# Kernel tuning notes

Hardware: AMD Instinct MI355X
Metric: run time of the kernel (lower is better)

Reference implementation:

```python
import jax, jax.numpy as jnp
import numpy as np

B, N, C, H, K = 4, 8192, 512, 8, 256
D = C // H  # head_dim = 64
EPS = 1e-6


def setup_inputs() -> dict:
    key = jax.random.key(0)
    k1, k2, k3 = jax.random.split(key, 3)
    x = jax.random.normal(k1, (B, N, C), dtype=jnp.float32)
    # Dense kernel (Keras default glorot-ish scale approximated; exact init irrelevant for math check)
    w_qkvv = jax.random.normal(k2, (C, 4 * C), dtype=jnp.float32) * (1.0 / np.sqrt(C))
    # UniformSqrtDim: uniform(-1/sqrt(K), 1/sqrt(K)) over shape (N, K)
    lim = 1.0 / np.sqrt(K)
    spatial_proj = jax.random.uniform(k3, (N, K), minval=-lim, maxval=lim, dtype=jnp.float32)
    temp_ca = jnp.ones((H, 1, 1), dtype=jnp.float32)
    temp_sa = jnp.ones((H, 1, 1), dtype=jnp.float32)
    return {"x": x, "w_qkvv": w_qkvv, "spatial_proj": spatial_proj,
            "temp_ca": temp_ca, "temp_sa": temp_sa}


def _safe_normalize(t):
    # normalize along last axis with clamped squared-sum (matches safe_normalize)
    sq = jnp.sum(t * t, axis=-1, keepdims=True)
    sq = jnp.where(sq < EPS, EPS, sq)
    return t / jnp.sqrt(sq)


def reference(x, w_qkvv, spatial_proj, temp_ca, temp_sa):
    b, n, c = x.shape
    qkvv = x @ w_qkvv  # [B, N, 4C]
    qkvv = qkvv.reshape(b, n, 4, H, D).transpose(2, 0, 3, 1, 4)  # [4, B, H, N, D]
    q, k, v_ca, v_sa = qkvv[0], qkvv[1], qkvv[2], qkvv[3]
    # transpose to [B, H, D, N]; normalize along N (tokens)
    q_t = q.transpose(0, 1, 3, 2)
    k_t = k.transpose(0, 1, 3, 2)
    v_ca_t = v_ca.transpose(0, 1, 3, 2)
    v_sa_t = v_sa.transpose(0, 1, 3, 2)
    q_norm = _safe_normalize(q_t)  # [B, H, D, N]
    k_norm = _safe_normalize(k_t)

    # --- Channel attention: [B,H,D,D] over small head_dim ---
    attn_ca = jnp.einsum('bhdn,bhen->bhde', q_norm, k_norm) * temp_ca
    attn_ca = jax.nn.softmax(attn_ca, axis=-1)
    x_ca = jnp.einsum('bhde,bhen->bhdn', attn_ca, v_ca_t)  # [B,H,D,N]
    x_ca = x_ca.transpose(0, 3, 1, 2).reshape(b, n, c)  # [B,N,C]

    # --- Spatial attention with N->K token projection ---
    k_proj = jnp.einsum('bhdn,nk->bhdk', k_norm, spatial_proj)  # [B,H,D,K]
    v_proj = jnp.einsum('bhdn,nk->bhdk', v_sa_t, spatial_proj)  # [B,H,D,K]
    attn_sa = jnp.einsum('bhdn,bhdk->bhnk', q_norm, k_proj) * temp_sa  # [B,H,N,K]
    attn_sa = jax.nn.softmax(attn_sa, axis=-1)
    x_sa = jnp.einsum('bhnk,bhdk->bhnd', attn_sa, v_proj)  # [B,H,N,D]
    x_sa = x_sa.transpose(0, 2, 1, 3).reshape(b, n, c)

    return x_ca + x_sa
```

## Files before the change

### kernel.cpp

```cpp
#include <hip/hip_runtime.h>
#include <hip/hip_bf16.h>

#define BATCH 4
#define SEQ   8192
#define CH    512
#define NHEAD 8
#define HDIM  64
#define KTOK  256
#define FOURC 2048

typedef __attribute__((ext_vector_type(8))) short bf16x8;
typedef __attribute__((ext_vector_type(4))) float f32x4;

#define GLOAD_LDS16(g, l)                                                      \
  __builtin_amdgcn_global_load_lds(                                            \
      (const __attribute__((address_space(1))) void*)(g),                      \
      (__attribute__((address_space(3))) void*)(l), 16, 0, 0)

__device__ __forceinline__ ushort bf16bits(float f) {
  __hip_bfloat16 b = __float2bfloat16(f);
  return *reinterpret_cast<ushort*>(&b);
}
__device__ __forceinline__ uint packbf2(float lo, float hi) {
  return (uint)bf16bits(lo) | ((uint)bf16bits(hi) << 16);
}

__global__ __launch_bounds__(256) void k_wt(
    const float* __restrict__ W, __hip_bfloat16* __restrict__ Wt) {
  __shared__ float tile[32][33];
  const int bx = blockIdx.x * 32;
  const int by = blockIdx.y * 32;
  const int t = threadIdx.x;
  const int r = t >> 5, c = t & 31;
#pragma unroll
  for (int it = 0; it < 4; ++it)
    tile[r + it * 8][c] = W[(size_t)(by + r + it * 8) * FOURC + bx + c];
  __syncthreads();
#pragma unroll
  for (int it = 0; it < 4; ++it) {
    int n = r + it * 8;
    Wt[(size_t)(bx + n) * CH + by + c] = __float2bfloat16(tile[c][n]);
  }
}

__global__ __launch_bounds__(256) void k_pt(
    const float* __restrict__ P, __hip_bfloat16* __restrict__ Pt) {
  __shared__ float tile[32][33];
  const int n0 = blockIdx.x * 32, k0 = blockIdx.y * 32;
  const int t = threadIdx.x, r = t >> 5, c = t & 31;
#pragma unroll
  for (int i = 0; i < 4; ++i)
    tile[r + i * 8][c] = P[(size_t)(n0 + r + i * 8) * KTOK + k0 + c];
  __syncthreads();
#pragma unroll
  for (int i = 0; i < 4; ++i)
    Pt[(size_t)(k0 + r + i * 8) * SEQ + n0 + c] = __float2bfloat16(tile[c][r + i * 8]);
}

__global__ __launch_bounds__(256) void k_xbf(
    const float* __restrict__ X, __hip_bfloat16* __restrict__ Xb) {
  size_t i = ((size_t)blockIdx.x * 256 + threadIdx.x) * 8;
  float4 a = *reinterpret_cast<const float4*>(&X[i]);
  float4 b = *reinterpret_cast<const float4*>(&X[i + 4]);
  ushort tmp[8];
  tmp[0] = bf16bits(a.x); tmp[1] = bf16bits(a.y);
  tmp[2] = bf16bits(a.z); tmp[3] = bf16bits(a.w);
  tmp[4] = bf16bits(b.x); tmp[5] = bf16bits(b.y);
  tmp[6] = bf16bits(b.z); tmp[7] = bf16bits(b.w);
  *reinterpret_cast<uint4*>(&Xb[i]) = *reinterpret_cast<const uint4*>(tmp);
}

__global__ __launch_bounds__(256) void k_gemm_mfma(
    const __hip_bfloat16* __restrict__ Xb, const __hip_bfloat16* __restrict__ Wt,
    __hip_bfloat16* __restrict__ QKVV) {
  __shared__ __align__(16) __hip_bfloat16 As[128 * 32];
  __shared__ __align__(16) __hip_bfloat16 Bs[128 * 32];
  const int t = threadIdx.x;
  const int wid = t >> 6, lane = t & 63;
  const int bid = blockIdx.x;
  const int xcd = bid & 7;
  const int l = bid >> 3;
  const int bm = (xcd * 32 + (l >> 4)) * 128;
  const int bn = (l & 15) * 128;
  const int wr = wid >> 1, wc = wid & 1;
  const int lrow = lane & 15;
  const int lk = (((lane >> 4) ^ ((lrow >> 1) & 3))) * 8;
  const int srow = lane >> 2;
  const int sk8 = (((lane & 3) ^ ((lane >> 3) & 3))) * 8;
  f32x4 acc[4][4] = {};
  for (int k0 = 0; k0 < CH; k0 += 32) {
#pragma unroll
    for (int i = 0; i < 2; ++i) {
      const int c = wid * 2 + i;
      GLOAD_LDS16(&Xb[(size_t)(bm + c * 16 + srow) * CH + k0 + sk8], &As[c * 512]);
      GLOAD_LDS16(&Wt[(size_t)(bn + c * 16 + srow) * CH + k0 + sk8], &Bs[c * 512]);
    }
    __syncthreads();
    bf16x8 af[4], bfr[4];
#pragma unroll
    for (int i = 0; i < 4; ++i)
      af[i] = *reinterpret_cast<const bf16x8*>(&As[(wr * 64 + i * 16 + lrow) * 32 + lk]);
#pragma unroll
    for (int j = 0; j < 4; ++j)
      bfr[j] = *reinterpret_cast<const bf16x8*>(&Bs[(wc * 64 + j * 16 + lrow) * 32 + lk]);
#pragma unroll
    for (int i = 0; i < 4; ++i)
#pragma unroll
      for (int j = 0; j < 4; ++j)
        acc[i][j] = __builtin_amdgcn_mfma_f32_16x16x32_bf16(af[i], bfr[j], acc[i][j], 0, 0, 0);
    __syncthreads();
  }
  const int l4 = (lane >> 4) * 4;
#pragma unroll
  for (int i = 0; i < 4; ++i)
#pragma unroll
    for (int j = 0; j < 4; ++j) {
      int col = bn + wc * 64 + j * 16 + lrow;
#pragma unroll
      for (int r = 0; r < 4; ++r) {
        int row = bm + wr * 64 + i * 16 + l4 + r;
        QKVV[(size_t)row * FOURC + col] = __float2bfloat16(acc[i][j][r]);
      }
    }
}

__global__ __launch_bounds__(256) void k_finalize(
    const float* __restrict__ sumsq, float* __restrict__ invq, float* __restrict__ invk) {
  int i = blockIdx.x * 256 + threadIdx.x;
  if (i < 2048) {
    invq[i] = rsqrtf(fmaxf(sumsq[i], 1e-6f));
    invk[i] = rsqrtf(fmaxf(sumsq[2048 + i], 1e-6f));
  }
}

__global__ __launch_bounds__(256) void k_qkstats(
    const __hip_bfloat16* __restrict__ QKVV,
    const __hip_bfloat16* __restrict__ Pt,
    float* __restrict__ G, float* __restrict__ sumsq, float* __restrict__ raw) {
  __shared__ __hip_bfloat16 qT[64][40];
  __shared__ __hip_bfloat16 kT[64][40];
  __shared__ __hip_bfloat16 vT[64][40];
  __shared__ __hip_bfloat16 pT[256][40];
  __shared__ float red[32][64];
  const int bh = blockIdx.y, b = bh >> 3, h = bh & 7;
  const int nbase = blockIdx.x * 1024;
  const int t = threadIdx.x, w = t >> 6, lane = t & 63;
  const int l15 = lane & 15, g = lane >> 4;
  const int comp = w >> 1, kh = w & 1;
  const int srow = t >> 3, sdq = (t & 7) * 8;
  f32x4 acc[4][8] = {};
  f32x4 accg[4] = {};
  float sqq[8] = {}, sqk[8] = {};
  for (int n0 = nbase; n0 < nbase + 1024; n0 += 32) {
    size_t gb = (size_t)(b * SEQ + n0 + srow) * FOURC + h * HDIM + sdq;
    uint4 uq = *reinterpret_cast<const uint4*>(&QKVV[gb]);
    uint4 uk = *reinterpret_cast<const uint4*>(&QKVV[gb + CH]);
    uint4 uv = *reinterpret_cast<const uint4*>(&QKVV[gb + 3 * CH]);
    const __hip_bfloat16* hq = reinterpret_cast<const __hip_bfloat16*>(&uq);
    const __hip_bfloat16* hk = reinterpret_cast<const __hip_bfloat16*>(&uk);
    const __hip_bfloat16* hv = reinterpret_cast<const __hip_bfloat16*>(&uv);
#pragma unroll
    for (int j = 0; j < 8; ++j) {
      float fq = __bfloat162float(hq[j]);
      float fk = __bfloat162float(hk[j]);
      sqq[j] = fmaf(fq, fq, sqq[j]);
      sqk[j] = fmaf(fk, fk, sqk[j]);
      qT[sdq + j][srow] = hq[j];
      kT[sdq + j][srow] = hk[j];
      vT[sdq + j][srow] = hv[j];
    }
#pragma unroll
    for (int ps = 0; ps < 4; ++ps) {
      int k = ps * 64 + (t >> 2);
      int poff = (t & 3) * 8;
      *reinterpret_cast<uint4*>(&pT[k][poff]) =
          *reinterpret_cast<const uint4*>(&Pt[(size_t)k * SEQ + n0 + poff]);
    }
    __syncthreads();
    {
      bf16x8 Aq[4];
#pragma unroll
      for (int dt = 0; dt < 4; ++dt)
        Aq[dt] = *reinterpret_cast<const bf16x8*>(&qT[dt * 16 + l15][g * 8]);
      bf16x8 Bk = *reinterpret_cast<const bf16x8*>(&kT[w * 16 + l15][g * 8]);
#pragma unroll
      for (int dt = 0; dt < 4; ++dt)
        accg[dt] = __builtin_amdgcn_mfma_f32_16x16x32_bf16(Aq[dt], Bk, accg[dt], 0, 0, 0);
    }
    {
      bf16x8 A[4], B[8];
#pragma unroll
      for (int dt = 0; dt < 4; ++dt)
        A[dt] = comp ? *reinterpret_cast<const bf16x8*>(&vT[dt * 16 + l15][g * 8])
                     : *reinterpret_cast<const bf16x8*>(&kT[dt * 16 + l15][g * 8]);
#pragma unroll
      for (int kt = 0; kt < 8; ++kt)
        B[kt] = *reinterpret_cast<const bf16x8*>(&pT[(kh * 8 + kt) * 16 + l15][g * 8]);
#pragma unroll
      for (int dt = 0; dt < 4; ++dt)
#pragma unroll
        for (int kt = 0; kt < 8; ++kt)
          acc[dt][kt] = __builtin_amdgcn_mfma_f32_16x16x32_bf16(A[dt], B[kt], acc[dt][kt], 0, 0, 0);
    }
    __syncthreads();
  }
#pragma unroll
  for (int j = 0; j < 8; ++j) red[srow][sdq + j] = sqq[j];
  __syncthreads();
  if (t < 64) {
    float tot = 0.f;
#pragma unroll
    for (int r = 0; r < 32; ++r) tot += red[r][t];
    atomicAdd(&sumsq[bh * 64 + t], tot);
  }
  __syncthreads();
#pragma unroll
  for (int j = 0; j < 8; ++j) red[srow][sdq + j] = sqk[j];
  __syncthreads();
  if (t < 64) {
    float tot = 0.f;
#pragma unroll
    for (int r = 0; r < 32; ++r) tot += red[r][t];
    atomicAdd(&sumsq[2048 + bh * 64 + t], tot);
  }
  float* gp = G + (size_t)bh * 4096;
#pragma unroll
  for (int dt = 0; dt < 4; ++dt)
#pragma unroll
    for (int r = 0; r < 4; ++r)
      atomicAdd(&gp[(dt * 16 + g * 4 + r) * 64 + w * 16 + l15], accg[dt][r]);
  float* rp = raw + ((size_t)bh * 2 + comp) * (64 * 256);
#pragma unroll
  for (int dt = 0; dt < 4; ++dt)
#pragma unroll
    for (int kt = 0; kt < 8; ++kt)
#pragma unroll
      for (int r = 0; r < 4; ++r)
        atomicAdd(&rp[(dt * 16 + g * 4 + r) * 256 + (kh * 8 + kt) * 16 + l15],
                  acc[dt][kt][r]);
}

__global__ __launch_bounds__(64) void k_ca_softmax(
    float* __restrict__ G, const float* __restrict__ invq,
    const float* __restrict__ invk, const float* __restrict__ tca) {
  const int bh = blockIdx.x, h = bh & 7;
  const int d = threadIdx.x;
  float* row = G + (size_t)bh * 4096 + d * 64;
  const float s0 = invq[bh * 64 + d] * tca[h];
  float vals[64];
  float m = -3.0e38f;
#pragma unroll
  for (int e = 0; e < 64; ++e) {
    float v = row[e] * s0 * invk[bh * 64 + e];
    vals[e] = v;
    m = fmaxf(m, v);
  }
  float s = 0.f;
#pragma unroll
  for (int e = 0; e < 64; ++e) { vals[e] = __expf(vals[e] - m); s += vals[e]; }
  float r = 1.0f / s;
#pragma unroll
  for (int e = 0; e < 64; ++e) row[e] = vals[e] * r;
}

__global__ __launch_bounds__(256) void k_projfin(
    const float* __restrict__ raw, const float* __restrict__ invq,
    const float* __restrict__ invk, const float* __restrict__ tsa,
    __hip_bfloat16* __restrict__ kpT, __hip_bfloat16* __restrict__ vpT) {
  const int bh = blockIdx.x, h = bh & 7;
  const int t = threadIdx.x;
  __shared__ float tile[64][65];
  const float ts = tsa[h];
  const float* r0 = raw + (size_t)bh * 2 * 16384;
  for (int kc = 0; kc < 4; ++kc) {
    for (int i = t; i < 4096; i += 256) {
      int d = i >> 6, kk = i & 63;
      tile[d][kk] = r0[d * 256 + kc * 64 + kk];
    }
    __syncthreads();
    for (int i = t; i < 4096; i += 256) {
      int kk = i >> 6, d = i & 63;
      float sc = invq[bh * 64 + d] * invk[bh * 64 + d] * ts;
      kpT[(size_t)bh * 16384 + (kc * 64 + kk) * 64 + d] = __float2bfloat16(tile[d][kk] * sc);
    }
    __syncthreads();
  }
  const float* r1 = r0 + 16384;
  for (int i = t; i < 16384; i += 256)
    vpT[(size_t)bh * 16384 + i] = __float2bfloat16(r1[i]);
}

__global__ __launch_bounds__(256) void k_xout(
    const __hip_bfloat16* __restrict__ QKVV,
    const float* __restrict__ G,
    const __hip_bfloat16* __restrict__ kpT,
    const __hip_bfloat16* __restrict__ vpT,
    float* __restrict__ out) {
  __shared__ __hip_bfloat16 vs[64][264];
  __shared__ __hip_bfloat16 ps[4][16][264];
  __shared__ __hip_bfloat16 gs[64][72];
  const int bh = blockIdx.y, b = bh >> 3, h = bh & 7;
  const int nblk = blockIdx.x * 512;
  const int t = threadIdx.x, w = t >> 6, lane = t & 63;
  const int l15 = lane & 15, g = lane >> 4;
  for (int i = t; i < 2048; i += 256) {
    int d = i >> 5, k8 = (i & 31) * 8;
    *reinterpret_cast<uint4*>(&vs[d][k8]) =
        *reinterpret_cast<const uint4*>(&vpT[((size_t)bh * 64 + d) * 256 + k8]);
  }
  for (int i = t; i < 4096; i += 256)
    gs[i >> 6][i & 63] = __float2bfloat16(G[(size_t)bh * 4096 + i]);
  bf16x8 kA[2][16];
#pragma unroll
  for (int s = 0; s < 2; ++s)
#pragma unroll
    for (int f = 0; f < 16; ++f)
      kA[s][f] = *reinterpret_cast<const bf16x8*>(
          &kpT[((size_t)bh * 256 + f * 16 + l15) * 64 + s * 32 + g * 8]);
  __syncthreads();
  const __hip_bfloat16* qbase = QKVV + (size_t)b * SEQ * FOURC + h * HDIM;
  const __hip_bfloat16* vbase = qbase + 2 * CH;
  for (int c = w; c < 32; c += 4) {
    const int n0 = nblk + c * 16;
    bf16x8 qf[2], vf[2];
#pragma unroll
    for (int s = 0; s < 2; ++s) {
      qf[s] = *reinterpret_cast<const bf16x8*>(
          &qbase[(size_t)(n0 + l15) * FOURC + s * 32 + g * 8]);
      vf[s] = *reinterpret_cast<const bf16x8*>(
          &vbase[(size_t)(n0 + l15) * FOURC + s * 32 + g * 8]);
    }
    f32x4 o[4] = {};
#pragma unroll
    for (int dt = 0; dt < 4; ++dt) {
      bf16x8 g0 = *reinterpret_cast<const bf16x8*>(&gs[dt * 16 + l15][g * 8]);
      bf16x8 g1 = *reinterpret_cast<const bf16x8*>(&gs[dt * 16 + l15][32 + g * 8]);
      o[dt] = __builtin_amdgcn_mfma_f32_16x16x32_bf16(vf[0], g0, o[dt], 0, 0, 0);
      o[dt] = __builtin_amdgcn_mfma_f32_16x16x32_bf16(vf[1], g1, o[dt], 0, 0, 0);
    }
    f32x4 acc[16] = {};
#pragma unroll
    for (int f = 0; f < 16; ++f) {
      acc[f] = __builtin_amdgcn_mfma_f32_16x16x32_bf16(kA[0][f], qf[0], acc[f], 0, 0, 0);
      acc[f] = __builtin_amdgcn_mfma_f32_16x16x32_bf16(kA[1][f], qf[1], acc[f], 0, 0, 0);
    }
    float m = -3.0e38f;
#pragma unroll
    for (int f = 0; f < 16; ++f)
#pragma unroll
      for (int r = 0; r < 4; ++r) m = fmaxf(m, acc[f][r]);
    m = fmaxf(m, __shfl_xor(m, 16));
    m = fmaxf(m, __shfl_xor(m, 32));
    float sum = 0.f;
#pragma unroll
    for (int f = 0; f < 16; ++f)
#pragma unroll
      for (int r = 0; r < 4; ++r) {
        float e = __expf(acc[f][r] - m);
        acc[f][r] = e; sum += e;
      }
    sum += __shfl_xor(sum, 16);
    sum += __shfl_xor(sum, 32);
    const float rinv = 1.0f / sum;
#pragma unroll
    for (int f = 0; f < 16; ++f) {
      uint2 pw;
      pw.x = packbf2(acc[f][0] * rinv, acc[f][1] * rinv);
      pw.y = packbf2(acc[f][2] * rinv, acc[f][3] * rinv);
      *reinterpret_cast<uint2*>(&ps[w][l15][f * 16 + g * 4]) = pw;
    }
    __builtin_amdgcn_wave_barrier();
#pragma unroll
    for (int s = 0; s < 8; ++s) {
      bf16x8 pa = *reinterpret_cast<const bf16x8*>(&ps[w][l15][s * 32 + g * 8]);
#pragma unroll
      for (int dt = 0; dt < 4; ++dt) {
        bf16x8 vb = *reinterpret_cast<const bf16x8*>(&vs[dt * 16 + l15][s * 32 + g * 8]);
        o[dt] = __builtin_amdgcn_mfma_f32_16x16x32_bf16(pa, vb, o[dt], 0, 0, 0);
      }
    }
#pragma unroll
    for (int dt = 0; dt < 4; ++dt)
#pragma unroll
      for (int r = 0; r < 4; ++r) {
        size_t oo = ((size_t)(b * SEQ + n0 + g * 4 + r)) * CH + h * HDIM + dt * 16 + l15;
        out[oo] = o[dt][r];
      }
    __builtin_amdgcn_wave_barrier();
  }
}

extern "C" void kernel_launch(void* const* d_in, const int* in_sizes, int n_in,
                              void* d_out, int out_size, void* d_ws, size_t ws_size,
                              hipStream_t stream) {
  const float* x   = (const float*)d_in[0];
  const float* w   = (const float*)d_in[1];
  const float* sp  = (const float*)d_in[2];
  const float* tca = (const float*)d_in[3];
  const float* tsa = (const float*)d_in[4];
  float* out = (float*)d_out;
  char* ws = (char*)d_ws;

  __hip_bfloat16* qkvv = (__hip_bfloat16*)ws;
  __hip_bfloat16* wt   = (__hip_bfloat16*)(ws + 134217728);
  __hip_bfloat16* pt   = (__hip_bfloat16*)(ws + 136314880);
  __hip_bfloat16* xb   = (__hip_bfloat16*)(ws + 140509184);
  __hip_bfloat16* kpT  = (__hip_bfloat16*)(ws + 174063616);
  __hip_bfloat16* vpT  = (__hip_bfloat16*)(ws + 175112192);
  float* invq  = (float*)(ws + 176160768);
  float* invk  = (float*)(ws + 176168960);
  float* G     = (float*)(ws + 176177152);
  float* sumsq = (float*)(ws + 176701440);
  float* raw   = (float*)(ws + 176717824);

  hipMemsetAsync(G, 0, 524288 + 16384 + 4194304, stream);

  hipLaunchKernelGGL(k_wt, dim3(64, 16), dim3(256), 0, stream, w, wt);
  hipLaunchKernelGGL(k_pt, dim3(256, 8), dim3(256), 0, stream, sp, pt);
  hipLaunchKernelGGL(k_xbf, dim3(8192), dim3(256), 0, stream, x, xb);
  hipLaunchKernelGGL(k_gemm_mfma, dim3(4096), dim3(256), 0, stream, xb, wt, qkvv);
  hipLaunchKernelGGL(k_qkstats, dim3(8, 32), dim3(256), 0, stream, qkvv, pt, G, sumsq, raw);
  hipLaunchKernelGGL(k_finalize, dim3(8), dim3(256), 0, stream, sumsq, invq, invk);
  hipLaunchKernelGGL(k_ca_softmax, dim3(32), dim3(64), 0, stream, G, invq, invk, tca);
  hipLaunchKernelGGL(k_projfin, dim3(32), dim3(256), 0, stream, raw, invq, invk, tsa, kpT, vpT);
  hipLaunchKernelGGL(k_xout, dim3(16, 32), dim3(256), 0, stream, qkvv, G, kpT, vpT, out);
}
```

Before: 290.5 us.

## Double-buffer GEMM LDS loads, prefetch qkstats tiles, fuse epilogue kernels

The projection GEMM now uses two LDS buffers, issuing the next k-tile's global-to-LDS loads before computing on the current one, with manual waitcnt and barriers. The qkstats loop prefetches the next chunk of Q/K/V and projection rows into registers while the current chunk is processed. The finalize, channel-softmax and projection-finalize kernels are merged into one epilogue kernel that writes the softmax matrix as bf16, which k_xout then loads with vector loads. This removes two launches and overlaps memory latency with MFMA work, at the cost of more LDS and registers. The bf16 Gb buffer reuses the xb workspace region, which is only safe because xb is no longer read after the GEMM.

```diff
diff --git a/kernel.cpp b/kernel.cpp
--- a/kernel.cpp
+++ b/kernel.cpp
@@ -73,8 +73,8 @@
 __global__ __launch_bounds__(256) void k_gemm_mfma(
     const __hip_bfloat16* __restrict__ Xb, const __hip_bfloat16* __restrict__ Wt,
     __hip_bfloat16* __restrict__ QKVV) {
-  __shared__ __align__(16) __hip_bfloat16 As[128 * 32];
-  __shared__ __align__(16) __hip_bfloat16 Bs[128 * 32];
+  __shared__ __align__(16) __hip_bfloat16 As[2][128 * 32];
+  __shared__ __align__(16) __hip_bfloat16 Bs[2][128 * 32];
   const int t = threadIdx.x;
   const int wid = t >> 6, lane = t & 63;
   const int bid = blockIdx.x;
@@ -87,29 +87,48 @@
   const int lk = (((lane >> 4) ^ ((lrow >> 1) & 3))) * 8;
   const int srow = lane >> 2;
   const int sk8 = (((lane & 3) ^ ((lane >> 3) & 3))) * 8;
+  const int c0 = wid * 2, c1 = wid * 2 + 1;
   f32x4 acc[4][4] = {};
-  for (int k0 = 0; k0 < CH; k0 += 32) {
-#pragma unroll
-    for (int i = 0; i < 2; ++i) {
-      const int c = wid * 2 + i;
-      GLOAD_LDS16(&Xb[(size_t)(bm + c * 16 + srow) * CH + k0 + sk8], &As[c * 512]);
-      GLOAD_LDS16(&Wt[(size_t)(bn + c * 16 + srow) * CH + k0 + sk8], &Bs[c * 512]);
-    }
-    __syncthreads();
+
+#define STAGE(bufi, kk)                                                         \
+  do {                                                                          \
+    GLOAD_LDS16(&Xb[(size_t)(bm + c0 * 16 + srow) * CH + (kk) + sk8],           \
+                &As[bufi][c0 * 512]);                                           \
+    GLOAD_LDS16(&Wt[(size_t)(bn + c0 * 16 + srow) * CH + (kk) + sk8],           \
+                &Bs[bufi][c0 * 512]);                                           \
+    GLOAD_LDS16(&Xb[(size_t)(bm + c1 * 16 + srow) * CH + (kk) + sk8],           \
+                &As[bufi][c1 * 512]);                                           \
+    GLOAD_LDS16(&Wt[(size_t)(bn + c1 * 16 + srow) * CH + (kk) + sk8],           \
+                &Bs[bufi][c1 * 512]);                                           \
+  } while (0)
+
+  STAGE(0, 0);
+#pragma unroll 4
+  for (int kt = 0; kt < 16; ++kt) {
+    const int cur = kt & 1;
+    if (kt < 15) {
+      STAGE(cur ^ 1, (kt + 1) * 32);
+      asm volatile("s_waitcnt vmcnt(4)" ::: "memory");
+    } else {
+      asm volatile("s_waitcnt vmcnt(0)" ::: "memory");
+    }
+    __builtin_amdgcn_s_barrier();
     bf16x8 af[4], bfr[4];
 #pragma unroll
     for (int i = 0; i < 4; ++i)
-      af[i] = *reinterpret_cast<const bf16x8*>(&As[(wr * 64 + i * 16 + lrow) * 32 + lk]);
+      af[i] = *reinterpret_cast<const bf16x8*>(&As[cur][(wr * 64 + i * 16 + lrow) * 32 + lk]);
 #pragma unroll
     for (int j = 0; j < 4; ++j)
-      bfr[j] = *reinterpret_cast<const bf16x8*>(&Bs[(wc * 64 + j * 16 + lrow) * 32 + lk]);
+      bfr[j] = *reinterpret_cast<const bf16x8*>(&Bs[cur][(wc * 64 + j * 16 + lrow) * 32 + lk]);
 #pragma unroll
     for (int i = 0; i < 4; ++i)
 #pragma unroll
       for (int j = 0; j < 4; ++j)
         acc[i][j] = __builtin_amdgcn_mfma_f32_16x16x32_bf16(af[i], bfr[j], acc[i][j], 0, 0, 0);
-    __syncthreads();
-  }
+    asm volatile("s_waitcnt lgkmcnt(0)" ::: "memory");
+    __builtin_amdgcn_s_barrier();
+  }
+#undef STAGE
   const int l4 = (lane >> 4) * 4;
 #pragma unroll
   for (int i = 0; i < 4; ++i)
@@ -122,15 +141,6 @@
         QKVV[(size_t)row * FOURC + col] = __float2bfloat16(acc[i][j][r]);
       }
     }
-}
-
-__global__ __launch_bounds__(256) void k_finalize(
-    const float* __restrict__ sumsq, float* __restrict__ invq, float* __restrict__ invk) {
-  int i = blockIdx.x * 256 + threadIdx.x;
-  if (i < 2048) {
-    invq[i] = rsqrtf(fmaxf(sumsq[i], 1e-6f));
-    invk[i] = rsqrtf(fmaxf(sumsq[2048 + i], 1e-6f));
-  }
 }
 
 __global__ __launch_bounds__(256) void k_qkstats(
@@ -148,33 +158,51 @@
   const int l15 = lane & 15, g = lane >> 4;
   const int comp = w >> 1, kh = w & 1;
   const int srow = t >> 3, sdq = (t & 7) * 8;
+  const int prow = t >> 2, poff = (t & 3) * 8;
   f32x4 acc[4][8] = {};
   f32x4 accg[4] = {};
   float sqq[8] = {}, sqk[8] = {};
-  for (int n0 = nbase; n0 < nbase + 1024; n0 += 32) {
-    size_t gb = (size_t)(b * SEQ + n0 + srow) * FOURC + h * HDIM + sdq;
-    uint4 uq = *reinterpret_cast<const uint4*>(&QKVV[gb]);
-    uint4 uk = *reinterpret_cast<const uint4*>(&QKVV[gb + CH]);
-    uint4 uv = *reinterpret_cast<const uint4*>(&QKVV[gb + 3 * CH]);
-    const __hip_bfloat16* hq = reinterpret_cast<const __hip_bfloat16*>(&uq);
-    const __hip_bfloat16* hk = reinterpret_cast<const __hip_bfloat16*>(&uk);
-    const __hip_bfloat16* hv = reinterpret_cast<const __hip_bfloat16*>(&uv);
-#pragma unroll
-    for (int j = 0; j < 8; ++j) {
-      float fq = __bfloat162float(hq[j]);
-      float fk = __bfloat162float(hk[j]);
-      sqq[j] = fmaf(fq, fq, sqq[j]);
-      sqk[j] = fmaf(fk, fk, sqk[j]);
-      qT[sdq + j][srow] = hq[j];
-      kT[sdq + j][srow] = hk[j];
-      vT[sdq + j][srow] = hv[j];
-    }
-#pragma unroll
-    for (int ps = 0; ps < 4; ++ps) {
-      int k = ps * 64 + (t >> 2);
-      int poff = (t & 3) * 8;
-      *reinterpret_cast<uint4*>(&pT[k][poff]) =
-          *reinterpret_cast<const uint4*>(&Pt[(size_t)k * SEQ + n0 + poff]);
+  uint4 uq, uk, uv, up0, up1, up2, up3;
+  {
+    size_t gb = (size_t)(b * SEQ + nbase + srow) * FOURC + h * HDIM + sdq;
+    uq = *reinterpret_cast<const uint4*>(&QKVV[gb]);
+    uk = *reinterpret_cast<const uint4*>(&QKVV[gb + CH]);
+    uv = *reinterpret_cast<const uint4*>(&QKVV[gb + 3 * CH]);
+    up0 = *reinterpret_cast<const uint4*>(&Pt[(size_t)(0 * 64 + prow) * SEQ + nbase + poff]);
+    up1 = *reinterpret_cast<const uint4*>(&Pt[(size_t)(1 * 64 + prow) * SEQ + nbase + poff]);
+    up2 = *reinterpret_cast<const uint4*>(&Pt[(size_t)(2 * 64 + prow) * SEQ + nbase + poff]);
+    up3 = *reinterpret_cast<const uint4*>(&Pt[(size_t)(3 * 64 + prow) * SEQ + nbase + poff]);
+  }
+  for (int it = 0; it < 32; ++it) {
+    {
+      const __hip_bfloat16* hq = reinterpret_cast<const __hip_bfloat16*>(&uq);
+      const __hip_bfloat16* hk = reinterpret_cast<const __hip_bfloat16*>(&uk);
+      const __hip_bfloat16* hv = reinterpret_cast<const __hip_bfloat16*>(&uv);
+#pragma unroll
+      for (int j = 0; j < 8; ++j) {
+        float fq = __bfloat162float(hq[j]);
+        float fk = __bfloat162float(hk[j]);
+        sqq[j] = fmaf(fq, fq, sqq[j]);
+        sqk[j] = fmaf(fk, fk, sqk[j]);
+        qT[sdq + j][srow] = hq[j];
+        kT[sdq + j][srow] = hk[j];
+        vT[sdq + j][srow] = hv[j];
+      }
+      *reinterpret_cast<uint4*>(&pT[0 * 64 + prow][poff]) = up0;
+      *reinterpret_cast<uint4*>(&pT[1 * 64 + prow][poff]) = up1;
+      *reinterpret_cast<uint4*>(&pT[2 * 64 + prow][poff]) = up2;
+      *reinterpret_cast<uint4*>(&pT[3 * 64 + prow][poff]) = up3;
+    }
+    if (it < 31) {
+      const int nn = nbase + (it + 1) * 32;
+      size_t gb = (size_t)(b * SEQ + nn + srow) * FOURC + h * HDIM + sdq;
+      uq = *reinterpret_cast<const uint4*>(&QKVV[gb]);
+      uk = *reinterpret_cast<const uint4*>(&QKVV[gb + CH]);
+      uv = *reinterpret_cast<const uint4*>(&QKVV[gb + 3 * CH]);
+      up0 = *reinterpret_cast<const uint4*>(&Pt[(size_t)(0 * 64 + prow) * SEQ + nn + poff]);
+      up1 = *reinterpret_cast<const uint4*>(&Pt[(size_t)(1 * 64 + prow) * SEQ + nn + poff]);
+      up2 = *reinterpret_cast<const uint4*>(&Pt[(size_t)(2 * 64 + prow) * SEQ + nn + poff]);
+      up3 = *reinterpret_cast<const uint4*>(&Pt[(size_t)(3 * 64 + prow) * SEQ + nn + poff]);
     }
     __syncthreads();
     {
@@ -240,39 +268,43 @@
                   acc[dt][kt][r]);
 }
 
-__global__ __launch_bounds__(64) void k_ca_softmax(
-    float* __restrict__ G, const float* __restrict__ invq,
-    const float* __restrict__ invk, const float* __restrict__ tca) {
-  const int bh = blockIdx.x, h = bh & 7;
-  const int d = threadIdx.x;
-  float* row = G + (size_t)bh * 4096 + d * 64;
-  const float s0 = invq[bh * 64 + d] * tca[h];
-  float vals[64];
-  float m = -3.0e38f;
-#pragma unroll
-  for (int e = 0; e < 64; ++e) {
-    float v = row[e] * s0 * invk[bh * 64 + e];
-    vals[e] = v;
-    m = fmaxf(m, v);
-  }
-  float s = 0.f;
-#pragma unroll
-  for (int e = 0; e < 64; ++e) { vals[e] = __expf(vals[e] - m); s += vals[e]; }
-  float r = 1.0f / s;
-#pragma unroll
-  for (int e = 0; e < 64; ++e) row[e] = vals[e] * r;
-}
-
-__global__ __launch_bounds__(256) void k_projfin(
-    const float* __restrict__ raw, const float* __restrict__ invq,
-    const float* __restrict__ invk, const float* __restrict__ tsa,
+__global__ __launch_bounds__(256) void k_epi(
+    const float* __restrict__ sumsq, const float* __restrict__ G,
+    const float* __restrict__ raw, const float* __restrict__ tca,
+    const float* __restrict__ tsa, __hip_bfloat16* __restrict__ Gb,
     __hip_bfloat16* __restrict__ kpT, __hip_bfloat16* __restrict__ vpT) {
+  __shared__ float iqs[64], iks[64];
+  __shared__ float tile[64][65];
   const int bh = blockIdx.x, h = bh & 7;
   const int t = threadIdx.x;
-  __shared__ float tile[64][65];
+  if (t < 64) {
+    iqs[t] = rsqrtf(fmaxf(sumsq[bh * 64 + t], 1e-6f));
+    iks[t] = rsqrtf(fmaxf(sumsq[2048 + bh * 64 + t], 1e-6f));
+  }
+  __syncthreads();
+  if (t < 64) {
+    const float* row = G + (size_t)bh * 4096 + t * 64;
+    const float s0 = iqs[t] * tca[h];
+    float vals[64];
+    float m = -3.0e38f;
+#pragma unroll
+    for (int e = 0; e < 64; ++e) {
+      float v = row[e] * s0 * iks[e];
+      vals[e] = v;
+      m = fmaxf(m, v);
+    }
+    float s = 0.f;
+#pragma unroll
+    for (int e = 0; e < 64; ++e) { vals[e] = __expf(vals[e] - m); s += vals[e]; }
+    float r = 1.0f / s;
+#pragma unroll
+    for (int e = 0; e < 64; ++e)
+      Gb[(size_t)bh * 4096 + t * 64 + e] = __float2bfloat16(vals[e] * r);
+  }
   const float ts = tsa[h];
   const float* r0 = raw + (size_t)bh * 2 * 16384;
   for (int kc = 0; kc < 4; ++kc) {
+    __syncthreads();
     for (int i = t; i < 4096; i += 256) {
       int d = i >> 6, kk = i & 63;
       tile[d][kk] = r0[d * 256 + kc * 64 + kk];
@@ -280,10 +312,9 @@
     __syncthreads();
     for (int i = t; i < 4096; i += 256) {
       int kk = i >> 6, d = i & 63;
-      float sc = invq[bh * 64 + d] * invk[bh * 64 + d] * ts;
+      float sc = iqs[d] * iks[d] * ts;
       kpT[(size_t)bh * 16384 + (kc * 64 + kk) * 64 + d] = __float2bfloat16(tile[d][kk] * sc);
     }
-    __syncthreads();
   }
   const float* r1 = r0 + 16384;
   for (int i = t; i < 16384; i += 256)
@@ -292,7 +323,7 @@
 
 __global__ __launch_bounds__(256) void k_xout(
     const __hip_bfloat16* __restrict__ QKVV,
-    const float* __restrict__ G,
+    const __hip_bfloat16* __restrict__ Gb,
     const __hip_bfloat16* __restrict__ kpT,
     const __hip_bfloat16* __restrict__ vpT,
     float* __restrict__ out) {
@@ -308,8 +339,11 @@
     *reinterpret_cast<uint4*>(&vs[d][k8]) =
         *reinterpret_cast<const uint4*>(&vpT[((size_t)bh * 64 + d) * 256 + k8]);
   }
-  for (int i = t; i < 4096; i += 256)
-    gs[i >> 6][i & 63] = __float2bfloat16(G[(size_t)bh * 4096 + i]);
+  for (int i = t; i < 512; i += 256) {
+    int row = i >> 3, q = i & 7;
+    *reinterpret_cast<uint4*>(&gs[row][q * 8]) =
+        *reinterpret_cast<const uint4*>(&Gb[(size_t)bh * 4096 + row * 64 + q * 8]);
+  }
   bf16x8 kA[2][16];
 #pragma unroll
   for (int s = 0; s < 2; ++s)
@@ -405,10 +439,9 @@
   __hip_bfloat16* wt   = (__hip_bfloat16*)(ws + 134217728);
   __hip_bfloat16* pt   = (__hip_bfloat16*)(ws + 136314880);
   __hip_bfloat16* xb   = (__hip_bfloat16*)(ws + 140509184);
+  __hip_bfloat16* gb   = (__hip_bfloat16*)(ws + 140509184);
   __hip_bfloat16* kpT  = (__hip_bfloat16*)(ws + 174063616);
   __hip_bfloat16* vpT  = (__hip_bfloat16*)(ws + 175112192);
-  float* invq  = (float*)(ws + 176160768);
-  float* invk  = (float*)(ws + 176168960);
   float* G     = (float*)(ws + 176177152);
   float* sumsq = (float*)(ws + 176701440);
   float* raw   = (float*)(ws + 176717824);
@@ -420,8 +453,7 @@
   hipLaunchKernelGGL(k_xbf, dim3(8192), dim3(256), 0, stream, x, xb);
   hipLaunchKernelGGL(k_gemm_mfma, dim3(4096), dim3(256), 0, stream, xb, wt, qkvv);
   hipLaunchKernelGGL(k_qkstats, dim3(8, 32), dim3(256), 0, stream, qkvv, pt, G, sumsq, raw);
-  hipLaunchKernelGGL(k_finalize, dim3(8), dim3(256), 0, stream, sumsq, invq, invk);
-  hipLaunchKernelGGL(k_ca_softmax, dim3(32), dim3(64), 0, stream, G, invq, invk, tca);
-  hipLaunchKernelGGL(k_projfin, dim3(32), dim3(256), 0, stream, raw, invq, invk, tsa, kpT, vpT);
-  hipLaunchKernelGGL(k_xout, dim3(16, 32), dim3(256), 0, stream, qkvv, G, kpT, vpT, out);
-}
+  hipLaunchKernelGGL(k_epi, dim3(32), dim3(256), 0, stream, sumsq, G, raw, tca, tsa,
+                     gb, kpT, vpT);
+  hipLaunchKernelGGL(k_xout, dim3(16, 32), dim3(256), 0, stream, qkvv, gb, kpT, vpT, out);
+}
```

Measured after the change: 287.2 us. About the same (-1.1%).
